# Optimization experiments

Measured on AMD Instinct MI355X. Metric: run time of the kernel, lower is better.

## Reference

```python
import jax, jax.numpy as jnp
import numpy as np

N = 20000        # total nodes
E = 240000       # directed edges (avg in-degree 12); self-loops appended in reference
G = 50           # graphs in the batch
NPG = N // G     # nodes per graph
TD = 768         # text embedding dim
HC = 64          # hidden_channels
H = 8            # attention heads for conv1..conv3 (conv4 uses 1 head)
FD = 3 * HC * H + HC  # JK cat dim for num_layers=4
NEG = 0.2        # GATv2 leaky_relu negative slope
EPS = 1e-5       # GraphNorm eps


def setup_inputs() -> dict:
    key = jax.random.key(0)
    ks = iter(jax.random.split(key, 64))

    def w(shape, s=0.05):
        return jax.random.normal(next(ks), shape, dtype=jnp.float32) * s

    z = lambda *s: jnp.zeros(s, jnp.float32)
    o = lambda *s: jnp.ones(s, jnp.float32)

    inp = {
        'x': w((N, TD), 1.0),
        'edge_index': jax.random.randint(next(ks), (2, E), 0, N, dtype=jnp.int32),
        'batch': jnp.arange(N, dtype=jnp.int32) // NPG,
        'ptr': jnp.arange(G + 1, dtype=jnp.int32) * NPG,
        'tp_w': w((TD, HC)), 'tp_b': z(HC),
        'lin_w': w((FD, 1), 0.005), 'lin_b': z(1),
    }
    # GATv2Conv params: lin_l (source), lin_r (target), att, output bias
    for name, ind, heads, concat in [('c1', HC, H, True), ('c2', HC * H, H, True),
                                     ('c3', HC * H, H, True), ('c4', HC * H, 1, False)]:
        inp[name + '_wl'] = w((ind, heads * HC)); inp[name + '_bl'] = z(heads * HC)
        inp[name + '_wr'] = w((ind, heads * HC)); inp[name + '_br'] = z(heads * HC)
        inp[name + '_att'] = w((heads, HC))
        inp[name + '_bias'] = z(heads * HC if concat else HC)
    # GraphNorm params: weight, bias, mean_scale
    for name, d in [('n1', HC * H), ('n2', HC * H), ('n3', HC * H), ('n4', HC)]:
        inp[name + '_w'] = o(d); inp[name + '_b'] = z(d); inp[name + '_ms'] = o(d)
    return inp


def _gatv2(x, src, dst, wl, bl, wr, br, att, bias, heads, concat):
    # GATv2: e_ij = att . leaky_relu(W_l x_j + W_r x_i); alpha = softmax over in-neighbors of i
    xl = (x @ wl + bl).reshape(N, heads, HC)
    xr = (x @ wr + br).reshape(N, heads, HC)
    e = jax.nn.leaky_relu(xl[src] + xr[dst], NEG)           # [E', H, C]
    logit = jnp.einsum('ehc,hc->eh', e, att)                # [E', H]
    m = jax.ops.segment_max(logit, dst, num_segments=N)     # stable scatter-softmax
    p = jnp.exp(logit - m[dst])
    alpha = p / jax.ops.segment_sum(p, dst, num_segments=N)[dst]
    out = jax.ops.segment_sum(xl[src] * alpha[..., None], dst, num_segments=N)
    out = out.reshape(N, heads * HC) if concat else out.mean(axis=1)
    return out + bias


def _gnorm(x, batch, w, b, ms):
    # PyG GraphNorm: per-graph mean (scaled by mean_scale), per-graph std
    cnt = jax.ops.segment_sum(jnp.ones((N,), x.dtype), batch, num_segments=G)[:, None]
    mean = jax.ops.segment_sum(x, batch, num_segments=G) / cnt
    cen = x - ms * mean[batch]
    var = jax.ops.segment_sum(cen * cen, batch, num_segments=G) / cnt
    return w * cen / jnp.sqrt(var + EPS)[batch] + b


def reference(x, tp_w, tp_b,
              c1_wl, c1_bl, c1_wr, c1_br, c1_att, c1_bias,
              c2_wl, c2_bl, c2_wr, c2_br, c2_att, c2_bias,
              c3_wl, c3_bl, c3_wr, c3_br, c3_att, c3_bias,
              c4_wl, c4_bl, c4_wr, c4_br, c4_att, c4_bias,
              n1_w, n1_b, n1_ms, n2_w, n2_b, n2_ms,
              n3_w, n3_b, n3_ms, n4_w, n4_b, n4_ms,
              lin_w, lin_b, edge_index, batch, ptr):
    sl = jnp.arange(N, dtype=edge_index.dtype)
    src = jnp.concatenate([edge_index[0], sl])  # add_self_loops=True
    dst = jnp.concatenate([edge_index[1], sl])

    h = x @ tp_w + tp_b                          # text_proj (dropout = identity in eval)
    h = _gatv2(h, src, dst, c1_wl, c1_bl, c1_wr, c1_br, c1_att, c1_bias, H, True)
    h = jax.nn.elu(_gnorm(h, batch, n1_w, n1_b, n1_ms))
    xs = [h]
    h2 = _gatv2(h, src, dst, c2_wl, c2_bl, c2_wr, c2_br, c2_att, c2_bias, H, True)
    h = jax.nn.elu(_gnorm(h2 + h, batch, n2_w, n2_b, n2_ms))
    xs.append(h)
    h3 = _gatv2(h, src, dst, c3_wl, c3_bl, c3_wr, c3_br, c3_att, c3_bias, H, True)
    h = jax.nn.elu(_gnorm(h3 + h, batch, n3_w, n3_b, n3_ms))
    xs.append(h)
    h = _gnorm(_gatv2(h, src, dst, c4_wl, c4_bl, c4_wr, c4_br, c4_att, c4_bias, 1, False),
               batch, n4_w, n4_b, n4_ms)
    xs.append(h)

    xcat = jnp.concatenate(xs, axis=1)           # JumpingKnowledge cat -> [N, FD]
    out = xcat[ptr[:-1]] @ lin_w + lin_b         # summary node per graph -> [G, 1]
    return out.squeeze(-1)                       # num_classes==2 -> squeeze
```

## Files before the change

### kernel.cpp

```cpp
#include <hip/hip_runtime.h>
#include <hip/hip_bf16.h>

#define NEG_SLOPE 0.2f
#define EPSI 1e-5f
#define THR 8.0f

typedef __attribute__((ext_vector_type(8))) short bf16x8;
typedef __attribute__((ext_vector_type(4))) float f32x4;

__device__ __forceinline__ float wred_sum(float v){
#pragma unroll
  for (int o = 32; o > 0; o >>= 1) v += __shfl_xor(v, o);
  return v;
}

__device__ __forceinline__ unsigned short f2bf(float f){
  __hip_bfloat16 h = __float2bfloat16(f);
  return *reinterpret_cast<unsigned short*>(&h);
}
__device__ __forceinline__ float bf2f(unsigned short u){
  return __uint_as_float((unsigned int)u << 16);
}

__device__ __forceinline__ void gload16(const void* g, void* l){
  __builtin_amdgcn_global_load_lds((const __attribute__((address_space(1))) unsigned int*)g,
                                   (__attribute__((address_space(3))) unsigned int*)l, 16, 0, 0);
}

__global__ __launch_bounds__(256) void k_count(const int* __restrict__ ei, int* __restrict__ deg,
                                               int E, int EP){
  int e = blockIdx.x * 256 + threadIdx.x;
  if (e >= EP) return;
  int d = (e < E) ? ei[E + e] : (e - E);
  atomicAdd(&deg[d], 1);
}

__global__ __launch_bounds__(256) void k_scan(const int* __restrict__ deg, int* __restrict__ rowptr, int n){
  __shared__ int part[256];
  int t = threadIdx.x;
  int L = (n + 255) / 256;
  int lo = t * L, hi = min(lo + L, n);
  int s = 0;
  for (int i = lo; i < hi; i++) s += deg[i];
  part[t] = s;
  __syncthreads();
  if (t == 0){
    int acc = 0;
    for (int i = 0; i < 256; i++){ int v = part[i]; part[i] = acc; acc += v; }
  }
  __syncthreads();
  int acc = part[t];
  for (int i = lo; i < hi; i++){ rowptr[i] = acc; acc += deg[i]; }
  if (t == 255) rowptr[n] = acc;
}

__global__ __launch_bounds__(256) void k_copy(const int* __restrict__ a, int* __restrict__ b, int n){
  int i = blockIdx.x * 256 + threadIdx.x;
  if (i < n) b[i] = a[i];
}

__global__ __launch_bounds__(256) void k_fill(const int* __restrict__ ei, int* __restrict__ cursor,
                                              int* __restrict__ srcn, int E, int EP){
  int e = blockIdx.x * 256 + threadIdx.x;
  if (e >= EP) return;
  int s, d;
  if (e < E){ s = ei[e]; d = ei[E + e]; } else { s = d = e - E; }
  int pos = atomicAdd(&cursor[d], 1);
  srcn[pos] = s;
}

__global__ __launch_bounds__(256) void k_cvt_act(const float* __restrict__ in,
                                                 unsigned short* __restrict__ ob, int total4){
  int i = blockIdx.x * 256 + threadIdx.x;
  if (i >= total4) return;
  float4 v = ((const float4*)in)[i];
  ushort4 o;
  o.x = f2bf(v.x); o.y = f2bf(v.y); o.z = f2bf(v.z); o.w = f2bf(v.w);
  ((ushort4*)ob)[i] = o;
}

__global__ __launch_bounds__(256) void k_cvt_wt(const float* __restrict__ W,
                                                unsigned short* __restrict__ Wt,
                                                int K, int Ncol){
  __shared__ float t[32][33];
  int bx = blockIdx.x, by = blockIdx.y;
  int tx = threadIdx.x & 31, ty = threadIdx.x >> 5;
#pragma unroll
  for (int i = 0; i < 4; i++)
    t[ty + i * 8][tx] = W[(size_t)(by * 32 + ty + i * 8) * Ncol + bx * 32 + tx];
  __syncthreads();
#pragma unroll
  for (int i = 0; i < 4; i++)
    Wt[(size_t)(bx * 32 + ty + i * 8) * K + by * 32 + tx] = f2bf(t[tx][ty + i * 8]);
}

__global__ __launch_bounds__(256) void k_catb(const float* __restrict__ a,
                                              const float* __restrict__ b,
                                              float* __restrict__ o, int n){
  int i = blockIdx.x * 256 + threadIdx.x;
  if (i < n) o[i] = a[i];
  else if (i < 2 * n) o[i] = b[i - n];
}

template<int BN>
__global__ __launch_bounds__(256) void k_gemm_mfma_t(const unsigned short* __restrict__ A,
                                                     const unsigned short* __restrict__ Wt,
                                                     const float* __restrict__ bias,
                                                     unsigned short* __restrict__ Cb,
                                                     int M, int K, int Ncol){
  constexpr int NF = BN / 32;
  __shared__ unsigned short As[128 * 32];
  __shared__ unsigned short Bs[BN * 32];
  const int tid = threadIdx.x;
  const int w = tid >> 6, lane = tid & 63;
  const int wr = w >> 1, wc = w & 1;
  const int row0 = blockIdx.y * 128, col0 = blockIdx.x * BN;
  const int lr = lane & 15, lk = lane >> 4;
  const int swz = (lr >> 1) & 3;

  f32x4 acc[4][NF];
#pragma unroll
  for (int i = 0; i < 4; i++)
#pragma unroll
    for (int j = 0; j < NF; j++) acc[i][j] = (f32x4){0.f, 0.f, 0.f, 0.f};

  for (int k0 = 0; k0 < K; k0 += 32){
#pragma unroll
    for (int c = 0; c < 2; c++){
      int g = w * 128 + c * 64 + lane;
      int row = g >> 2, slot = g & 3;
      int kq = slot ^ ((row >> 1) & 3);
      int srow = row0 + row; if (srow >= M) srow = M - 1;
      gload16(&A[(size_t)srow * K + k0 + kq * 8], &As[(size_t)(w * 128 + c * 64) * 8]);
    }
#pragma unroll
    for (int c = 0; c < BN / 64; c++){
      int g = w * BN + c * 64 + lane;
      int col = g >> 2, slot = g & 3;
      int kq = slot ^ ((col >> 1) & 3);
      gload16(&Wt[(size_t)(col0 + col) * K + k0 + kq * 8], &Bs[(size_t)(w * BN + c * 64) * 8]);
    }
    __syncthreads();

    bf16x8 af[4], bf_[NF];
#pragma unroll
    for (int mi = 0; mi < 4; mi++){
      int rl = wr * 64 + mi * 16 + lr;
      af[mi] = *(const bf16x8*)&As[(rl * 4 + (lk ^ swz)) * 8];
    }
#pragma unroll
    for (int ni = 0; ni < NF; ni++){
      int cl = wc * (BN / 2) + ni * 16 + lr;
      bf_[ni] = *(const bf16x8*)&Bs[(cl * 4 + (lk ^ swz)) * 8];
    }
#pragma unroll
    for (int mi = 0; mi < 4; mi++)
#pragma unroll
      for (int ni = 0; ni < NF; ni++)
        acc[mi][ni] = __builtin_amdgcn_mfma_f32_16x16x32_bf16(af[mi], bf_[ni], acc[mi][ni], 0, 0, 0);
    __syncthreads();
  }

#pragma unroll
  for (int mi = 0; mi < 4; mi++){
#pragma unroll
    for (int ni = 0; ni < NF; ni++){
      int gc = col0 + wc * (BN / 2) + ni * 16 + lr;
      float bv = bias[gc];
#pragma unroll
      for (int r = 0; r < 4; r++){
        int gr = row0 + wr * 64 + mi * 16 + lk * 4 + r;
        if (gr < M) Cb[(size_t)gr * Ncol + gc] = f2bf(acc[mi][ni][r] + bv);
      }
    }
  }
}

__global__ __launch_bounds__(256) void k_gat_fused8(const unsigned short* __restrict__ xlrb,
                                                    const float* __restrict__ att,
                                                    const int* __restrict__ rowptr,
                                                    const int* __restrict__ srcn,
                                                    const float* __restrict__ bias,
                                                    const unsigned short* __restrict__ resb,
                                                    float* __restrict__ out,
                                                    int N){
  int node = (blockIdx.x * 256 + threadIdx.x) >> 6;
  int lane = threadIdx.x & 63;
  if (node >= N) return;
  float xr[8], av[8];
  {
    bf16x8 r8 = *(const bf16x8*)&xlrb[(size_t)node * 1024 + 512 + lane * 8];
    float4 a0 = *(const float4*)&att[lane * 8];
    float4 a1 = *(const float4*)&att[lane * 8 + 4];
#pragma unroll
    for (int j = 0; j < 8; j++) xr[j] = bf2f((unsigned short)r8[j]);
    av[0] = a0.x; av[1] = a0.y; av[2] = a0.z; av[3] = a0.w;
    av[4] = a1.x; av[5] = a1.y; av[6] = a1.z; av[7] = a1.w;
  }
  int e0 = rowptr[node], e1 = rowptr[node + 1];
  float m0 = -1e30f, s0 = 0.f, m1 = -1e30f, s1 = 0.f;
  float acc0[8] = {}, acc1[8] = {};

  for (int base = e0; base < e1; base += 64){
    int cnt = min(64, e1 - base);
    int sn = 0;
    if (lane < cnt) sn = srcn[base + lane];
    int k = 0;
    for (; k + 1 < cnt; k += 2){
      int ska = __shfl(sn, k);
      int skb = __shfl(sn, k + 1);
      bf16x8 va8 = *(const bf16x8*)&xlrb[(size_t)ska * 1024 + lane * 8];
      bf16x8 vb8 = *(const bf16x8*)&xlrb[(size_t)skb * 1024 + lane * 8];
      float va[8], vb[8];
#pragma unroll
      for (int j = 0; j < 8; j++){ va[j] = bf2f((unsigned short)va8[j]); vb[j] = bf2f((unsigned short)vb8[j]); }
      float suma = 0.f, sumb = 0.f;
#pragma unroll
      for (int j = 0; j < 8; j++){
        float ta = va[j] + xr[j]; ta = ta > 0.f ? ta : NEG_SLOPE * ta; suma += ta * av[j];
        float tb = vb[j] + xr[j]; tb = tb > 0.f ? tb : NEG_SLOPE * tb; sumb += tb * av[j];
      }
      suma += __shfl_xor(suma, 1); sumb += __shfl_xor(sumb, 1);
      suma += __shfl_xor(suma, 2); sumb += __shfl_xor(sumb, 2);
      suma += __shfl_xor(suma, 4); sumb += __shfl_xor(sumb, 4);
      if (__builtin_expect(__any(suma > m0 + THR), 0)){
        float mn = fmaxf(m0, suma);
        float cs = __expf(m0 - mn);
        float p  = __expf(suma - mn);
        s0 = s0 * cs + p;
#pragma unroll
        for (int j = 0; j < 8; j++) acc0[j] = acc0[j] * cs + p * va[j];
        m0 = mn;
      } else {
        float p = __expf(suma - m0);
        s0 += p;
#pragma unroll
        for (int j = 0; j < 8; j++) acc0[j] += p * va[j];
      }
      if (__builtin_expect(__any(sumb > m1 + THR), 0)){
        float mn = fmaxf(m1, sumb);
        float cs = __expf(m1 - mn);
        float p  = __expf(sumb - mn);
        s1 = s1 * cs + p;
#pragma unroll
        for (int j = 0; j < 8; j++) acc1[j] = acc1[j] * cs + p * vb[j];
        m1 = mn;
      } else {
        float p = __expf(sumb - m1);
        s1 += p;
#pragma unroll
        for (int j = 0; j < 8; j++) acc1[j] += p * vb[j];
      }
    }
    if (k < cnt){
      int ska = __shfl(sn, k);
      bf16x8 va8 = *(const bf16x8*)&xlrb[(size_t)ska * 1024 + lane * 8];
      float va[8];
#pragma unroll
      for (int j = 0; j < 8; j++) va[j] = bf2f((unsigned short)va8[j]);
      float suma = 0.f;
#pragma unroll
      for (int j = 0; j < 8; j++){
        float ta = va[j] + xr[j]; ta = ta > 0.f ? ta : NEG_SLOPE * ta; suma += ta * av[j];
      }
      suma += __shfl_xor(suma, 1);
      suma += __shfl_xor(suma, 2);
      suma += __shfl_xor(suma, 4);
      if (__builtin_expect(__any(suma > m0 + THR), 0)){
        float mn = fmaxf(m0, suma);
        float cs = __expf(m0 - mn);
        float p  = __expf(suma - mn);
        s0 = s0 * cs + p;
#pragma unroll
        for (int j = 0; j < 8; j++) acc0[j] = acc0[j] * cs + p * va[j];
        m0 = mn;
      } else {
        float p = __expf(suma - m0);
        s0 += p;
#pragma unroll
        for (int j = 0; j < 8; j++) acc0[j] += p * va[j];
      }
    }
  }
  float m = fmaxf(m0, m1);
  float c0 = __expf(m0 - m), c1 = __expf(m1 - m);
  float s = s0 * c0 + s1 * c1;
  float inv = 1.f / s;
  size_t o = (size_t)node * 512 + lane * 8;
  float4 bv0 = *(const float4*)&bias[lane * 8];
  float4 bv1 = *(const float4*)&bias[lane * 8 + 4];
  float rr[8] = {};
  if (resb){
    bf16x8 r8 = *(const bf16x8*)&resb[o];
#pragma unroll
    for (int j = 0; j < 8; j++) rr[j] = bf2f((unsigned short)r8[j]);
  }
  float bb[8] = {bv0.x, bv0.y, bv0.z, bv0.w, bv1.x, bv1.y, bv1.z, bv1.w};
  float4 o0, o1;
  float res8[8];
#pragma unroll
  for (int j = 0; j < 8; j++)
    res8[j] = (acc0[j] * c0 + acc1[j] * c1) * inv + bb[j] + rr[j];
  o0.x = res8[0]; o0.y = res8[1]; o0.z = res8[2]; o0.w = res8[3];
  o1.x = res8[4]; o1.y = res8[5]; o1.z = res8[6]; o1.w = res8[7];
  *(float4*)&out[o] = o0;
  *(float4*)&out[o + 4] = o1;
}

__global__ __launch_bounds__(256) void k_gat_fused1(const unsigned short* __restrict__ xlr,
                                                    const float* __restrict__ att,
                                                    const int* __restrict__ rowptr,
                                                    const int* __restrict__ srcn,
                                                    const float* __restrict__ bias,
                                                    float* __restrict__ out,
                                                    int N){
  int node = (blockIdx.x * 256 + threadIdx.x) >> 6;
  int lane = threadIdx.x & 63;
  if (node >= N) return;
  float xrv = bf2f(xlr[(size_t)node * 128 + 64 + lane]);
  float attv = att[lane];
  int e0 = rowptr[node], e1 = rowptr[node + 1];
  float m = -1e30f, s = 0.f, acc = 0.f;
  for (int base = e0; base < e1; base += 64){
    int cnt = min(64, e1 - base);
    int sn = 0;
    if (lane < cnt) sn = srcn[base + lane];
    for (int k = 0; k < cnt; k++){
      int sk = __shfl(sn, k);
      float v = bf2f(xlr[(size_t)sk * 128 + lane]);
      float t = v + xrv;
      t = t > 0.f ? t : NEG_SLOPE * t;
      float sum = wred_sum(t * attv);
      if (sum > m + THR){
        float mn = fmaxf(m, sum);
        float cs = __expf(m - mn);
        float p  = __expf(sum - mn);
        s = s * cs + p;
        acc = acc * cs + p * v;
        m = mn;
      } else {
        float p = __expf(sum - m);
        s += p;
        acc += p * v;
      }
    }
  }
  out[(size_t)node * 64 + lane] = acc / s + bias[lane];
}

#define NCHUNK 16
__global__ __launch_bounds__(256) void k_gnorm_stats(const float* __restrict__ y,
                                                     const int* __restrict__ ptrg,
                                                     float* __restrict__ psum,
                                                     float* __restrict__ psq,
                                                     int OD){
  int g = blockIdx.x, chunk = blockIdx.z;
  int lane = threadIdx.x & 63, sub = threadIdx.x >> 6;
  int c = blockIdx.y * 64 + lane;
  int lo = ptrg[g], hi = ptrg[g + 1], len = hi - lo;
  int c0 = lo + (len * chunk) / NCHUNK, c1 = lo + (len * (chunk + 1)) / NCHUNK;
  float s = 0.f, q = 0.f;
  for (int i = c0 + sub; i < c1; i += 4){
    float v = y[(size_t)i * OD + c];
    s += v; q += v * v;
  }
  __shared__ float sm[4][64], sq2[4][64];
  sm[sub][lane] = s; sq2[sub][lane] = q;
  __syncthreads();
  if (sub == 0){
    s = sm[0][lane] + sm[1][lane] + sm[2][lane] + sm[3][lane];
    q = sq2[0][lane] + sq2[1][lane] + sq2[2][lane] + sq2[3][lane];
    size_t o = (size_t)(g * NCHUNK + chunk) * OD + c;
    psum[o] = s; psq[o] = q;
  }
}

__global__ __launch_bounds__(256) void k_gnorm_coef(const float* __restrict__ psum,
                                                    const float* __restrict__ psq,
                                                    const float* __restrict__ w,
                                                    const float* __restrict__ b,
                                                    const float* __restrict__ ms,
                                                    const int* __restrict__ ptrg,
                                                    float* __restrict__ cA,
                                                    float* __restrict__ cC,
                                                    int OD){
  int g = blockIdx.x;
  int len = ptrg[g + 1] - ptrg[g];
  float inv_n = 1.f / (float)len;
  for (int c = threadIdx.x; c < OD; c += 256){
    float s = 0.f, q = 0.f;
    for (int k = 0; k < NCHUNK; k++){
      size_t o = (size_t)(g * NCHUNK + k) * OD + c;
      s += psum[o]; q += psq[o];
    }
    float mean = s * inv_n, ey2 = q * inv_n;
    float m = ms[c];
    float var = ey2 - mean * mean * (2.f * m - m * m);
    float inv = rsqrtf(var + EPSI);
    float A = w[c] * inv;
    cA[(size_t)g * OD + c] = A;
    cC[(size_t)g * OD + c] = b[c] - A * m * mean;
  }
}

__global__ __launch_bounds__(256) void k_gnorm_apply(const float* __restrict__ y,
                                                     const int* __restrict__ batch,
                                                     const float* __restrict__ cA,
                                                     const float* __restrict__ cC,
                                                     unsigned short* __restrict__ outb,
                                                     int OD, int total4, int do_elu){
  int idx = blockIdx.x * 256 + threadIdx.x;
  if (idx >= total4) return;
  int od4 = OD >> 2;
  int node = idx / od4;
  int c = (idx - node * od4) << 2;
  int g = batch[node];
  float4 v = ((const float4*)y)[idx];
  float4 A = *(const float4*)&cA[(size_t)g * OD + c];
  float4 Cc = *(const float4*)&cC[(size_t)g * OD + c];
  float4 r;
  r.x = A.x * v.x + Cc.x;
  r.y = A.y * v.y + Cc.y;
  r.z = A.z * v.z + Cc.z;
  r.w = A.w * v.w + Cc.w;
  if (do_elu){
    r.x = r.x > 0.f ? r.x : expf(r.x) - 1.f;
    r.y = r.y > 0.f ? r.y : expf(r.y) - 1.f;
    r.z = r.z > 0.f ? r.z : expf(r.z) - 1.f;
    r.w = r.w > 0.f ? r.w : expf(r.w) - 1.f;
  }
  ushort4 ob;
  ob.x = f2bf(r.x); ob.y = f2bf(r.y); ob.z = f2bf(r.z); ob.w = f2bf(r.w);
  ((ushort4*)outb)[idx] = ob;
}

__global__ __launch_bounds__(64) void k_extract(const unsigned short* __restrict__ srcb,
                                                float* __restrict__ cat,
                                                const int* __restrict__ ptrg,
                                                int OD, int off, int FD){
  int g = blockIdx.x;
  int c = blockIdx.y * 64 + threadIdx.x;
  cat[(size_t)g * FD + off + c] = bf2f(srcb[(size_t)ptrg[g] * OD + c]);
}

__global__ __launch_bounds__(256) void k_final(const float* __restrict__ cat,
                                               const float* __restrict__ lin_w,
                                               const float* __restrict__ lin_b,
                                               float* __restrict__ out, int FD){
  int g = blockIdx.x;
  float s = 0.f;
  for (int c = threadIdx.x; c < FD; c += 256) s += cat[(size_t)g * FD + c] * lin_w[c];
  s = wred_sum(s);
  __shared__ float sm[4];
  if ((threadIdx.x & 63) == 0) sm[threadIdx.x >> 6] = s;
  __syncthreads();
  if (threadIdx.x == 0) out[g] = sm[0] + sm[1] + sm[2] + sm[3] + lin_b[0];
}

extern "C" void kernel_launch(void* const* d_in, const int* in_sizes, int n_in,
                              void* d_out, int out_size, void* d_ws, size_t ws_size,
                              hipStream_t stream) {
  const int TD = 768, HC = 64, H = 8;
  const float* x     = (const float*)d_in[0];
  const int*   ei    = (const int*)d_in[1];
  const int*   batch = (const int*)d_in[2];
  const int*   ptrg  = (const int*)d_in[3];
  const float* tp_w  = (const float*)d_in[4];
  const float* tp_b  = (const float*)d_in[5];
  const float* lin_w = (const float*)d_in[6];
  const float* lin_b = (const float*)d_in[7];
  const float* cw[4][6];
  for (int l = 0; l < 4; l++)
    for (int j = 0; j < 6; j++) cw[l][j] = (const float*)d_in[8 + 6 * l + j];
  const float* nw[4][3];
  for (int l = 0; l < 4; l++)
    for (int j = 0; j < 3; j++) nw[l][j] = (const float*)d_in[32 + 3 * l + j];

  const int N  = in_sizes[0] / TD;
  const int E  = in_sizes[1] / 2;
  const int EP = E + N;
  const int G  = in_sizes[3] - 1;
  const int FD = 3 * HC * H + HC;

  char* wsp = (char*)d_ws;
  size_t off = 0;
  auto alloc = [&](size_t b) -> void* {
    void* p = wsp + off;
    off += (b + 255) & ~(size_t)255;
    return p;
  };
  float* tmpF  = (float*)alloc((size_t)N * 512 * 4);
  unsigned short* xlrb = (unsigned short*)alloc((size_t)N * 1024 * 2);
  unsigned short* actA = (unsigned short*)alloc((size_t)N * 512 * 2);
  unsigned short* h0h  = (unsigned short*)alloc((size_t)N * 64 * 2);
  int*   rowptr= (int*)alloc((size_t)(N + 1) * 4);
  int*   cursor= (int*)alloc((size_t)N * 4);
  int*   srcn  = (int*)alloc((size_t)EP * 4);
  float* cat   = (float*)alloc((size_t)G * FD * 4);
  float* psum  = (float*)alloc((size_t)G * NCHUNK * 512 * 4);
  float* psq   = (float*)alloc((size_t)G * NCHUNK * 512 * 4);
  float* cA    = (float*)alloc((size_t)G * 512 * 4);
  float* cC    = (float*)alloc((size_t)G * 512 * 4);
  unsigned short* WtLR = (unsigned short*)alloc((size_t)1024 * 512 * 2);
  unsigned short* WtTP = (unsigned short*)alloc((size_t)64 * 768 * 2);
  unsigned short* Wt4  = (unsigned short*)alloc((size_t)128 * 512 * 2);
  float* cbias = (float*)alloc(1024 * 4);
  (void)ws_size; (void)n_in; (void)out_size;

  float* out = (float*)d_out;

  unsigned short* xbf   = xlrb;
  unsigned short* xlr4b = xlrb;
  float* agg4 = tmpF;

  hipMemsetAsync(cursor, 0, (size_t)N * 4, stream);
  int eblk = (EP + 255) / 256;
  k_count<<<eblk, 256, 0, stream>>>(ei, cursor, E, EP);
  k_scan<<<1, 256, 0, stream>>>(cursor, rowptr, N);
  k_copy<<<(N + 255) / 256, 256, 0, stream>>>(rowptr, cursor, N);
  k_fill<<<eblk, 256, 0, stream>>>(ei, cursor, srcn, E, EP);

  const int mfmaRows = (N + 127) / 128;
  const int nodeBlocks = (N + 3) / 4;

  k_cvt_act<<<(N * TD / 4 + 255) / 256, 256, 0, stream>>>(x, xbf, N * TD / 4);
  k_cvt_wt<<<dim3(2, TD / 32), 256, 0, stream>>>(tp_w, WtTP, TD, 64);
  k_gemm_mfma_t<64><<<dim3(1, mfmaRows), 256, 0, stream>>>(xbf, WtTP, tp_b, h0h, N, TD, 64);

  auto layer8 = [&](const unsigned short* actbf, int Kin, int l,
                    const unsigned short* resb, unsigned short* youtb, int catoff){
    k_cvt_wt<<<dim3(16, Kin / 32), 256, 0, stream>>>(cw[l][0], WtLR, Kin, 512);
    k_cvt_wt<<<dim3(16, Kin / 32), 256, 0, stream>>>(cw[l][2], WtLR + (size_t)512 * Kin, Kin, 512);
    k_catb<<<4, 256, 0, stream>>>(cw[l][1], cw[l][3], cbias, 512);
    k_gemm_mfma_t<128><<<dim3(8, mfmaRows), 256, 0, stream>>>(actbf, WtLR, cbias, xlrb, N, Kin, 1024);
    k_gat_fused8<<<nodeBlocks, 256, 0, stream>>>(xlrb, cw[l][4], rowptr, srcn,
                                                 cw[l][5], resb, tmpF, N);
    k_gnorm_stats<<<dim3(G, 8, NCHUNK), 256, 0, stream>>>(tmpF, ptrg, psum, psq, 512);
    k_gnorm_coef<<<G, 256, 0, stream>>>(psum, psq, nw[l][0], nw[l][1], nw[l][2], ptrg, cA, cC, 512);
    int total4 = N * 128;
    k_gnorm_apply<<<(total4 + 255) / 256, 256, 0, stream>>>(tmpF, batch, cA, cC, youtb,
                                                            512, total4, 1);
    k_extract<<<dim3(G, 8), 64, 0, stream>>>(youtb, cat, ptrg, 512, catoff, FD);
  };

  layer8(h0h,  64,  0, nullptr, actA, 0);
  layer8(actA, 512, 1, actA,    actA, 512);
  layer8(actA, 512, 2, actA,    actA, 1024);

  k_cvt_wt<<<dim3(2, 16), 256, 0, stream>>>(cw[3][0], Wt4, 512, 64);
  k_cvt_wt<<<dim3(2, 16), 256, 0, stream>>>(cw[3][2], Wt4 + (size_t)64 * 512, 512, 64);
  k_catb<<<1, 256, 0, stream>>>(cw[3][1], cw[3][3], cbias, 64);
  k_gemm_mfma_t<64><<<dim3(2, mfmaRows), 256, 0, stream>>>(actA, Wt4, cbias, xlr4b, N, 512, 128);
  k_gat_fused1<<<nodeBlocks, 256, 0, stream>>>(xlr4b, cw[3][4], rowptr, srcn,
                                               cw[3][5], agg4, N);
  k_gnorm_stats<<<dim3(G, 1, NCHUNK), 256, 0, stream>>>(agg4, ptrg, psum, psq, 64);
  k_gnorm_coef<<<G, 256, 0, stream>>>(psum, psq, nw[3][0], nw[3][1], nw[3][2], ptrg, cA, cC, 64);
  k_gnorm_apply<<<(N * 16 + 255) / 256, 256, 0, stream>>>(agg4, batch, cA, cC, h0h,
                                                          64, N * 16, 0);
  k_extract<<<dim3(G, 1), 64, 0, stream>>>(h0h, cat, ptrg, 64, 1536, FD);

  k_final<<<G, 256, 0, stream>>>(cat, lin_w, lin_b, out, FD);
}
```

Measured before the change: 551.2 us.

## Store GAT outputs in bf16, fuse small kernels, widen GEMM tiles, pack math

The GAT aggregation output now goes to bf16 instead of fp32, which halves the traffic through the GraphNorm stats and apply passes. Several small launches are removed: the k_copy pass is folded into the scan, the two weight conversions and the bias concat are merged, and the summary-node extract is folded into gnorm apply. The GEMM moves to 512-thread blocks with wider N tiles and reads its two biases directly. The GAT inner loop uses packed float2 math and a max-based leaky ReLU. Rounding the pre-norm activations to bf16 adds precision loss before the normalization statistics are computed.

```diff
diff --git a/kernel.cpp b/kernel.cpp
--- a/kernel.cpp
+++ b/kernel.cpp
@@ -7,6 +7,7 @@
 
 typedef __attribute__((ext_vector_type(8))) short bf16x8;
 typedef __attribute__((ext_vector_type(4))) float f32x4;
+typedef __attribute__((ext_vector_type(2))) float f32x2;
 
 __device__ __forceinline__ float wred_sum(float v){
 #pragma unroll
@@ -20,6 +21,19 @@
 }
 __device__ __forceinline__ float bf2f(unsigned short u){
   return __uint_as_float((unsigned int)u << 16);
+}
+__device__ __forceinline__ f32x2 bfpair(unsigned int u){
+  f32x2 r;
+  r.x = __uint_as_float(u << 16);
+  r.y = __uint_as_float(u & 0xffff0000u);
+  return r;
+}
+__device__ __forceinline__ f32x2 vmax2(f32x2 a, f32x2 b){
+#if __has_builtin(__builtin_elementwise_max)
+  return __builtin_elementwise_max(a, b);
+#else
+  f32x2 r; r.x = fmaxf(a.x, b.x); r.y = fmaxf(a.y, b.y); return r;
+#endif
 }
 
 __device__ __forceinline__ void gload16(const void* g, void* l){
@@ -35,7 +49,7 @@
   atomicAdd(&deg[d], 1);
 }
 
-__global__ __launch_bounds__(256) void k_scan(const int* __restrict__ deg, int* __restrict__ rowptr, int n){
+__global__ __launch_bounds__(256) void k_scan(int* __restrict__ deg, int* __restrict__ rowptr, int n){
   __shared__ int part[256];
   int t = threadIdx.x;
   int L = (n + 255) / 256;
@@ -50,13 +64,13 @@
   }
   __syncthreads();
   int acc = part[t];
-  for (int i = lo; i < hi; i++){ rowptr[i] = acc; acc += deg[i]; }
+  for (int i = lo; i < hi; i++){
+    int d = deg[i];
+    rowptr[i] = acc;
+    deg[i] = acc;
+    acc += d;
+  }
   if (t == 255) rowptr[n] = acc;
-}
-
-__global__ __launch_bounds__(256) void k_copy(const int* __restrict__ a, int* __restrict__ b, int n){
-  int i = blockIdx.x * 256 + threadIdx.x;
-  if (i < n) b[i] = a[i];
 }
 
 __global__ __launch_bounds__(256) void k_fill(const int* __restrict__ ei, int* __restrict__ cursor,
@@ -94,26 +108,41 @@
     Wt[(size_t)(bx * 32 + ty + i * 8) * K + by * 32 + tx] = f2bf(t[tx][ty + i * 8]);
 }
 
-__global__ __launch_bounds__(256) void k_catb(const float* __restrict__ a,
-                                              const float* __restrict__ b,
-                                              float* __restrict__ o, int n){
-  int i = blockIdx.x * 256 + threadIdx.x;
-  if (i < n) o[i] = a[i];
-  else if (i < 2 * n) o[i] = b[i - n];
+__global__ __launch_bounds__(256) void k_cvt_wt2(const float* __restrict__ Wa,
+                                                 const float* __restrict__ Wb,
+                                                 unsigned short* __restrict__ Wt,
+                                                 int K, int Ncol){
+  __shared__ float t[32][33];
+  int half = gridDim.x >> 1;
+  int isB = blockIdx.x >= half;
+  const float* W = isB ? Wb : Wa;
+  unsigned short* out = Wt + (isB ? (size_t)Ncol * K : 0);
+  int bx = isB ? blockIdx.x - half : blockIdx.x;
+  int by = blockIdx.y;
+  int tx = threadIdx.x & 31, ty = threadIdx.x >> 5;
+#pragma unroll
+  for (int i = 0; i < 4; i++)
+    t[ty + i * 8][tx] = W[(size_t)(by * 32 + ty + i * 8) * Ncol + bx * 32 + tx];
+  __syncthreads();
+#pragma unroll
+  for (int i = 0; i < 4; i++)
+    out[(size_t)(bx * 32 + ty + i * 8) * K + by * 32 + tx] = f2bf(t[tx][ty + i * 8]);
 }
 
 template<int BN>
-__global__ __launch_bounds__(256) void k_gemm_mfma_t(const unsigned short* __restrict__ A,
-                                                     const unsigned short* __restrict__ Wt,
-                                                     const float* __restrict__ bias,
-                                                     unsigned short* __restrict__ Cb,
-                                                     int M, int K, int Ncol){
-  constexpr int NF = BN / 32;
+__global__ __launch_bounds__(512) void k_gemm_mfma8(const unsigned short* __restrict__ A,
+                                                    const unsigned short* __restrict__ Wt,
+                                                    const float* __restrict__ ba,
+                                                    const float* __restrict__ bb,
+                                                    int bsplit,
+                                                    unsigned short* __restrict__ Cb,
+                                                    int M, int K, int Ncol){
+  constexpr int NF = BN / 64;
   __shared__ unsigned short As[128 * 32];
   __shared__ unsigned short Bs[BN * 32];
   const int tid = threadIdx.x;
   const int w = tid >> 6, lane = tid & 63;
-  const int wr = w >> 1, wc = w & 1;
+  const int wr = w >> 2, wc = w & 3;
   const int row0 = blockIdx.y * 128, col0 = blockIdx.x * BN;
   const int lr = lane & 15, lk = lane >> 4;
   const int swz = (lr >> 1) & 3;
@@ -125,20 +154,18 @@
     for (int j = 0; j < NF; j++) acc[i][j] = (f32x4){0.f, 0.f, 0.f, 0.f};
 
   for (int k0 = 0; k0 < K; k0 += 32){
-#pragma unroll
-    for (int c = 0; c < 2; c++){
-      int g = w * 128 + c * 64 + lane;
+    for (int g0 = w * 64; g0 < 512; g0 += 512){
+      int g = g0 + lane;
       int row = g >> 2, slot = g & 3;
       int kq = slot ^ ((row >> 1) & 3);
       int srow = row0 + row; if (srow >= M) srow = M - 1;
-      gload16(&A[(size_t)srow * K + k0 + kq * 8], &As[(size_t)(w * 128 + c * 64) * 8]);
-    }
-#pragma unroll
-    for (int c = 0; c < BN / 64; c++){
-      int g = w * BN + c * 64 + lane;
+      gload16(&A[(size_t)srow * K + k0 + kq * 8], &As[(size_t)g0 * 8]);
+    }
+    for (int g0 = w * 64; g0 < BN * 4; g0 += 512){
+      int g = g0 + lane;
       int col = g >> 2, slot = g & 3;
       int kq = slot ^ ((col >> 1) & 3);
-      gload16(&Wt[(size_t)(col0 + col) * K + k0 + kq * 8], &Bs[(size_t)(w * BN + c * 64) * 8]);
+      gload16(&Wt[(size_t)(col0 + col) * K + k0 + kq * 8], &Bs[(size_t)g0 * 8]);
     }
     __syncthreads();
 
@@ -150,7 +177,7 @@
     }
 #pragma unroll
     for (int ni = 0; ni < NF; ni++){
-      int cl = wc * (BN / 2) + ni * 16 + lr;
+      int cl = wc * (BN / 4) + ni * 16 + lr;
       bf_[ni] = *(const bf16x8*)&Bs[(cl * 4 + (lk ^ swz)) * 8];
     }
 #pragma unroll
@@ -165,8 +192,8 @@
   for (int mi = 0; mi < 4; mi++){
 #pragma unroll
     for (int ni = 0; ni < NF; ni++){
-      int gc = col0 + wc * (BN / 2) + ni * 16 + lr;
-      float bv = bias[gc];
+      int gc = col0 + wc * (BN / 4) + ni * 16 + lr;
+      float bv = gc < bsplit ? ba[gc] : bb[gc - bsplit];
 #pragma unroll
       for (int r = 0; r < 4; r++){
         int gr = row0 + wr * 64 + mi * 16 + lk * 4 + r;
@@ -182,24 +209,23 @@
                                                     const int* __restrict__ srcn,
                                                     const float* __restrict__ bias,
                                                     const unsigned short* __restrict__ resb,
-                                                    float* __restrict__ out,
+                                                    unsigned short* __restrict__ yb,
                                                     int N){
   int node = (blockIdx.x * 256 + threadIdx.x) >> 6;
   int lane = threadIdx.x & 63;
   if (node >= N) return;
-  float xr[8], av[8];
+  f32x2 xr2[4], av2[4];
   {
-    bf16x8 r8 = *(const bf16x8*)&xlrb[(size_t)node * 1024 + 512 + lane * 8];
+    uint4 ur = *(const uint4*)&xlrb[(size_t)node * 1024 + 512 + lane * 8];
+    xr2[0] = bfpair(ur.x); xr2[1] = bfpair(ur.y); xr2[2] = bfpair(ur.z); xr2[3] = bfpair(ur.w);
     float4 a0 = *(const float4*)&att[lane * 8];
     float4 a1 = *(const float4*)&att[lane * 8 + 4];
-#pragma unroll
-    for (int j = 0; j < 8; j++) xr[j] = bf2f((unsigned short)r8[j]);
-    av[0] = a0.x; av[1] = a0.y; av[2] = a0.z; av[3] = a0.w;
-    av[4] = a1.x; av[5] = a1.y; av[6] = a1.z; av[7] = a1.w;
+    av2[0] = (f32x2){a0.x, a0.y}; av2[1] = (f32x2){a0.z, a0.w};
+    av2[2] = (f32x2){a1.x, a1.y}; av2[3] = (f32x2){a1.z, a1.w};
   }
   int e0 = rowptr[node], e1 = rowptr[node + 1];
   float m0 = -1e30f, s0 = 0.f, m1 = -1e30f, s1 = 0.f;
-  float acc0[8] = {}, acc1[8] = {};
+  f32x2 acc0[4] = {}, acc1[4] = {};
 
   for (int base = e0; base < e1; base += 64){
     int cnt = min(64, e1 - base);
@@ -209,17 +235,22 @@
     for (; k + 1 < cnt; k += 2){
       int ska = __shfl(sn, k);
       int skb = __shfl(sn, k + 1);
-      bf16x8 va8 = *(const bf16x8*)&xlrb[(size_t)ska * 1024 + lane * 8];
-      bf16x8 vb8 = *(const bf16x8*)&xlrb[(size_t)skb * 1024 + lane * 8];
-      float va[8], vb[8];
-#pragma unroll
-      for (int j = 0; j < 8; j++){ va[j] = bf2f((unsigned short)va8[j]); vb[j] = bf2f((unsigned short)vb8[j]); }
-      float suma = 0.f, sumb = 0.f;
-#pragma unroll
-      for (int j = 0; j < 8; j++){
-        float ta = va[j] + xr[j]; ta = ta > 0.f ? ta : NEG_SLOPE * ta; suma += ta * av[j];
-        float tb = vb[j] + xr[j]; tb = tb > 0.f ? tb : NEG_SLOPE * tb; sumb += tb * av[j];
-      }
+      uint4 ua = *(const uint4*)&xlrb[(size_t)ska * 1024 + lane * 8];
+      uint4 ub = *(const uint4*)&xlrb[(size_t)skb * 1024 + lane * 8];
+      f32x2 va[4], vb[4];
+      va[0] = bfpair(ua.x); va[1] = bfpair(ua.y); va[2] = bfpair(ua.z); va[3] = bfpair(ua.w);
+      vb[0] = bfpair(ub.x); vb[1] = bfpair(ub.y); vb[2] = bfpair(ub.z); vb[3] = bfpair(ub.w);
+      f32x2 da = (f32x2){0.f, 0.f}, db = (f32x2){0.f, 0.f};
+#pragma unroll
+      for (int j = 0; j < 4; j++){
+        f32x2 ta = va[j] + xr2[j];
+        f32x2 tb = vb[j] + xr2[j];
+        ta = vmax2(ta, ta * NEG_SLOPE);
+        tb = vmax2(tb, tb * NEG_SLOPE);
+        da += ta * av2[j];
+        db += tb * av2[j];
+      }
+      float suma = da.x + da.y, sumb = db.x + db.y;
       suma += __shfl_xor(suma, 1); sumb += __shfl_xor(sumb, 1);
       suma += __shfl_xor(suma, 2); sumb += __shfl_xor(sumb, 2);
       suma += __shfl_xor(suma, 4); sumb += __shfl_xor(sumb, 4);
@@ -229,13 +260,13 @@
         float p  = __expf(suma - mn);
         s0 = s0 * cs + p;
 #pragma unroll
-        for (int j = 0; j < 8; j++) acc0[j] = acc0[j] * cs + p * va[j];
+        for (int j = 0; j < 4; j++) acc0[j] = acc0[j] * cs + va[j] * p;
         m0 = mn;
       } else {
         float p = __expf(suma - m0);
         s0 += p;
 #pragma unroll
-        for (int j = 0; j < 8; j++) acc0[j] += p * va[j];
+        for (int j = 0; j < 4; j++) acc0[j] += va[j] * p;
       }
       if (__builtin_expect(__any(sumb > m1 + THR), 0)){
         float mn = fmaxf(m1, sumb);
@@ -243,26 +274,28 @@
         float p  = __expf(sumb - mn);
         s1 = s1 * cs + p;
 #pragma unroll
-        for (int j = 0; j < 8; j++) acc1[j] = acc1[j] * cs + p * vb[j];
+        for (int j = 0; j < 4; j++) acc1[j] = acc1[j] * cs + vb[j] * p;
         m1 = mn;
       } else {
         float p = __expf(sumb - m1);
         s1 += p;
 #pragma unroll
-        for (int j = 0; j < 8; j++) acc1[j] += p * vb[j];
+        for (int j = 0; j < 4; j++) acc1[j] += vb[j] * p;
       }
     }
     if (k < cnt){
       int ska = __shfl(sn, k);
-      bf16x8 va8 = *(const bf16x8*)&xlrb[(size_t)ska * 1024 + lane * 8];
-      float va[8];
-#pragma unroll
-      for (int j = 0; j < 8; j++) va[j] = bf2f((unsigned short)va8[j]);
-      float suma = 0.f;
-#pragma unroll
-      for (int j = 0; j < 8; j++){
-        float ta = va[j] + xr[j]; ta = ta > 0.f ? ta : NEG_SLOPE * ta; suma += ta * av[j];
-      }
+      uint4 ua = *(const uint4*)&xlrb[(size_t)ska * 1024 + lane * 8];
+      f32x2 va[4];
+      va[0] = bfpair(ua.x); va[1] = bfpair(ua.y); va[2] = bfpair(ua.z); va[3] = bfpair(ua.w);
+      f32x2 da = (f32x2){0.f, 0.f};
+#pragma unroll
+      for (int j = 0; j < 4; j++){
+        f32x2 ta = va[j] + xr2[j];
+        ta = vmax2(ta, ta * NEG_SLOPE);
+        da += ta * av2[j];
+      }
+      float suma = da.x + da.y;
       suma += __shfl_xor(suma, 1);
       suma += __shfl_xor(suma, 2);
       suma += __shfl_xor(suma, 4);
@@ -272,13 +305,13 @@
         float p  = __expf(suma - mn);
         s0 = s0 * cs + p;
 #pragma unroll
-        for (int j = 0; j < 8; j++) acc0[j] = acc0[j] * cs + p * va[j];
+        for (int j = 0; j < 4; j++) acc0[j] = acc0[j] * cs + va[j] * p;
         m0 = mn;
       } else {
         float p = __expf(suma - m0);
         s0 += p;
 #pragma unroll
-        for (int j = 0; j < 8; j++) acc0[j] += p * va[j];
+        for (int j = 0; j < 4; j++) acc0[j] += va[j] * p;
       }
     }
   }
@@ -286,25 +319,24 @@
   float c0 = __expf(m0 - m), c1 = __expf(m1 - m);
   float s = s0 * c0 + s1 * c1;
   float inv = 1.f / s;
+  float4 b0 = *(const float4*)&bias[lane * 8];
+  float4 b1 = *(const float4*)&bias[lane * 8 + 4];
+  f32x2 bi2[4] = {(f32x2){b0.x, b0.y}, (f32x2){b0.z, b0.w},
+                  (f32x2){b1.x, b1.y}, (f32x2){b1.z, b1.w}};
+  f32x2 re2[4] = {};
   size_t o = (size_t)node * 512 + lane * 8;
-  float4 bv0 = *(const float4*)&bias[lane * 8];
-  float4 bv1 = *(const float4*)&bias[lane * 8 + 4];
-  float rr[8] = {};
   if (resb){
-    bf16x8 r8 = *(const bf16x8*)&resb[o];
-#pragma unroll
-    for (int j = 0; j < 8; j++) rr[j] = bf2f((unsigned short)r8[j]);
-  }
-  float bb[8] = {bv0.x, bv0.y, bv0.z, bv0.w, bv1.x, bv1.y, bv1.z, bv1.w};
-  float4 o0, o1;
-  float res8[8];
-#pragma unroll
-  for (int j = 0; j < 8; j++)
-    res8[j] = (acc0[j] * c0 + acc1[j] * c1) * inv + bb[j] + rr[j];
-  o0.x = res8[0]; o0.y = res8[1]; o0.z = res8[2]; o0.w = res8[3];
-  o1.x = res8[4]; o1.y = res8[5]; o1.z = res8[6]; o1.w = res8[7];
-  *(float4*)&out[o] = o0;
-  *(float4*)&out[o + 4] = o1;
+    uint4 rr = *(const uint4*)&resb[o];
+    re2[0] = bfpair(rr.x); re2[1] = bfpair(rr.y); re2[2] = bfpair(rr.z); re2[3] = bfpair(rr.w);
+  }
+  bf16x8 ov;
+#pragma unroll
+  for (int j = 0; j < 4; j++){
+    f32x2 r = (acc0[j] * c0 + acc1[j] * c1) * inv + bi2[j] + re2[j];
+    ov[2 * j]     = (short)f2bf(r.x);
+    ov[2 * j + 1] = (short)f2bf(r.y);
+  }
+  *(bf16x8*)&yb[o] = ov;
 }
 
 __global__ __launch_bounds__(256) void k_gat_fused1(const unsigned short* __restrict__ xlr,
@@ -312,7 +344,7 @@
                                                     const int* __restrict__ rowptr,
                                                     const int* __restrict__ srcn,
                                                     const float* __restrict__ bias,
-                                                    float* __restrict__ out,
+                                                    unsigned short* __restrict__ yb4,
                                                     int N){
   int node = (blockIdx.x * 256 + threadIdx.x) >> 6;
   int lane = threadIdx.x & 63;
@@ -329,7 +361,7 @@
       int sk = __shfl(sn, k);
       float v = bf2f(xlr[(size_t)sk * 128 + lane]);
       float t = v + xrv;
-      t = t > 0.f ? t : NEG_SLOPE * t;
+      t = fmaxf(t, t * NEG_SLOPE);
       float sum = wred_sum(t * attv);
       if (sum > m + THR){
         float mn = fmaxf(m, sum);
@@ -345,11 +377,11 @@
       }
     }
   }
-  out[(size_t)node * 64 + lane] = acc / s + bias[lane];
+  yb4[(size_t)node * 64 + lane] = f2bf(acc / s + bias[lane]);
 }
 
 #define NCHUNK 16
-__global__ __launch_bounds__(256) void k_gnorm_stats(const float* __restrict__ y,
+__global__ __launch_bounds__(256) void k_gnorm_stats(const unsigned short* __restrict__ y,
                                                      const int* __restrict__ ptrg,
                                                      float* __restrict__ psum,
                                                      float* __restrict__ psq,
@@ -361,7 +393,7 @@
   int c0 = lo + (len * chunk) / NCHUNK, c1 = lo + (len * (chunk + 1)) / NCHUNK;
   float s = 0.f, q = 0.f;
   for (int i = c0 + sub; i < c1; i += 4){
-    float v = y[(size_t)i * OD + c];
+    float v = bf2f(y[(size_t)i * OD + c]);
     s += v; q += v * v;
   }
   __shared__ float sm[4][64], sq2[4][64];
@@ -403,11 +435,14 @@
   }
 }
 
-__global__ __launch_bounds__(256) void k_gnorm_apply(const float* __restrict__ y,
+__global__ __launch_bounds__(256) void k_gnorm_apply(const unsigned short* __restrict__ y,
                                                      const int* __restrict__ batch,
                                                      const float* __restrict__ cA,
                                                      const float* __restrict__ cC,
                                                      unsigned short* __restrict__ outb,
+                                                     const int* __restrict__ ptrg,
+                                                     float* __restrict__ cat,
+                                                     int catoff, int FD,
                                                      int OD, int total4, int do_elu){
   int idx = blockIdx.x * 256 + threadIdx.x;
   if (idx >= total4) return;
@@ -415,7 +450,8 @@
   int node = idx / od4;
   int c = (idx - node * od4) << 2;
   int g = batch[node];
-  float4 v = ((const float4*)y)[idx];
+  ushort4 uv = ((const ushort4*)y)[idx];
+  float4 v = make_float4(bf2f(uv.x), bf2f(uv.y), bf2f(uv.z), bf2f(uv.w));
   float4 A = *(const float4*)&cA[(size_t)g * OD + c];
   float4 Cc = *(const float4*)&cC[(size_t)g * OD + c];
   float4 r;
@@ -432,15 +468,8 @@
   ushort4 ob;
   ob.x = f2bf(r.x); ob.y = f2bf(r.y); ob.z = f2bf(r.z); ob.w = f2bf(r.w);
   ((ushort4*)outb)[idx] = ob;
-}
-
-__global__ __launch_bounds__(64) void k_extract(const unsigned short* __restrict__ srcb,
-                                                float* __restrict__ cat,
-                                                const int* __restrict__ ptrg,
-                                                int OD, int off, int FD){
-  int g = blockIdx.x;
-  int c = blockIdx.y * 64 + threadIdx.x;
-  cat[(size_t)g * FD + off + c] = bf2f(srcb[(size_t)ptrg[g] * OD + c]);
+  if (node == ptrg[g])
+    *(float4*)&cat[(size_t)g * FD + catoff + c] = r;
 }
 
 __global__ __launch_bounds__(256) void k_final(const float* __restrict__ cat,
@@ -489,8 +518,8 @@
     off += (b + 255) & ~(size_t)255;
     return p;
   };
-  float* tmpF  = (float*)alloc((size_t)N * 512 * 4);
   unsigned short* xlrb = (unsigned short*)alloc((size_t)N * 1024 * 2);
+  unsigned short* yb   = (unsigned short*)alloc((size_t)N * 512 * 2);
   unsigned short* actA = (unsigned short*)alloc((size_t)N * 512 * 2);
   unsigned short* h0h  = (unsigned short*)alloc((size_t)N * 64 * 2);
   int*   rowptr= (int*)alloc((size_t)(N + 1) * 4);
@@ -504,20 +533,18 @@
   unsigned short* WtLR = (unsigned short*)alloc((size_t)1024 * 512 * 2);
   unsigned short* WtTP = (unsigned short*)alloc((size_t)64 * 768 * 2);
   unsigned short* Wt4  = (unsigned short*)alloc((size_t)128 * 512 * 2);
-  float* cbias = (float*)alloc(1024 * 4);
   (void)ws_size; (void)n_in; (void)out_size;
 
   float* out = (float*)d_out;
 
   unsigned short* xbf   = xlrb;
   unsigned short* xlr4b = xlrb;
-  float* agg4 = tmpF;
+  unsigned short* yb4   = yb;
 
   hipMemsetAsync(cursor, 0, (size_t)N * 4, stream);
   int eblk = (EP + 255) / 256;
   k_count<<<eblk, 256, 0, stream>>>(ei, cursor, E, EP);
   k_scan<<<1, 256, 0, stream>>>(cursor, rowptr, N);
-  k_copy<<<(N + 255) / 256, 256, 0, stream>>>(rowptr, cursor, N);
   k_fill<<<eblk, 256, 0, stream>>>(ei, cursor, srcn, E, EP);
 
   const int mfmaRows = (N + 127) / 128;
@@ -525,39 +552,37 @@
 
   k_cvt_act<<<(N * TD / 4 + 255) / 256, 256, 0, stream>>>(x, xbf, N * TD / 4);
   k_cvt_wt<<<dim3(2, TD / 32), 256, 0, stream>>>(tp_w, WtTP, TD, 64);
-  k_gemm_mfma_t<64><<<dim3(1, mfmaRows), 256, 0, stream>>>(xbf, WtTP, tp_b, h0h, N, TD, 64);
+  k_gemm_mfma8<64><<<dim3(1, mfmaRows), 512, 0, stream>>>(xbf, WtTP, tp_b, tp_b, 64, h0h, N, TD, 64);
 
   auto layer8 = [&](const unsigned short* actbf, int Kin, int l,
-                    const unsigned short* resb, unsigned short* youtb, int catoff){
-    k_cvt_wt<<<dim3(16, Kin / 32), 256, 0, stream>>>(cw[l][0], WtLR, Kin, 512);
-    k_cvt_wt<<<dim3(16, Kin / 32), 256, 0, stream>>>(cw[l][2], WtLR + (size_t)512 * Kin, Kin, 512);
-    k_catb<<<4, 256, 0, stream>>>(cw[l][1], cw[l][3], cbias, 512);
-    k_gemm_mfma_t<128><<<dim3(8, mfmaRows), 256, 0, stream>>>(actbf, WtLR, cbias, xlrb, N, Kin, 1024);
+                    const unsigned short* resb, int catoff){
+    k_cvt_wt2<<<dim3(32, Kin / 32), 256, 0, stream>>>(cw[l][0], cw[l][2], WtLR, Kin, 512);
+    k_gemm_mfma8<256><<<dim3(4, mfmaRows), 512, 0, stream>>>(actbf, WtLR, cw[l][1], cw[l][3], 512,
+                                                             xlrb, N, Kin, 1024);
     k_gat_fused8<<<nodeBlocks, 256, 0, stream>>>(xlrb, cw[l][4], rowptr, srcn,
-                                                 cw[l][5], resb, tmpF, N);
-    k_gnorm_stats<<<dim3(G, 8, NCHUNK), 256, 0, stream>>>(tmpF, ptrg, psum, psq, 512);
+                                                 cw[l][5], resb, yb, N);
+    k_gnorm_stats<<<dim3(G, 8, NCHUNK), 256, 0, stream>>>(yb, ptrg, psum, psq, 512);
     k_gnorm_coef<<<G, 256, 0, stream>>>(psum, psq, nw[l][0], nw[l][1], nw[l][2], ptrg, cA, cC, 512);
     int total4 = N * 128;
-    k_gnorm_apply<<<(total4 + 255) / 256, 256, 0, stream>>>(tmpF, batch, cA, cC, youtb,
+    k_gnorm_apply<<<(total4 + 255) / 256, 256, 0, stream>>>(yb, batch, cA, cC, actA,
+                                                            ptrg, cat, catoff, FD,
                                                             512, total4, 1);
-    k_extract<<<dim3(G, 8), 64, 0, stream>>>(youtb, cat, ptrg, 512, catoff, FD);
   };
 
-  layer8(h0h,  64,  0, nullptr, actA, 0);
-  layer8(actA, 512, 1, actA,    actA, 512);
-  layer8(actA, 512, 2, actA,    actA, 1024);
-
-  k_cvt_wt<<<dim3(2, 16), 256, 0, stream>>>(cw[3][0], Wt4, 512, 64);
-  k_cvt_wt<<<dim3(2, 16), 256, 0, stream>>>(cw[3][2], Wt4 + (size_t)64 * 512, 512, 64);
-  k_catb<<<1, 256, 0, stream>>>(cw[3][1], cw[3][3], cbias, 64);
-  k_gemm_mfma_t<64><<<dim3(2, mfmaRows), 256, 0, stream>>>(actA, Wt4, cbias, xlr4b, N, 512, 128);
+  layer8(h0h,  64,  0, nullptr, 0);
+  layer8(actA, 512, 1, actA,    512);
+  layer8(actA, 512, 2, actA,    1024);
+
+  k_cvt_wt2<<<dim3(4, 16), 256, 0, stream>>>(cw[3][0], cw[3][2], Wt4, 512, 64);
+  k_gemm_mfma8<128><<<dim3(1, mfmaRows), 512, 0, stream>>>(actA, Wt4, cw[3][1], cw[3][3], 64,
+                                                           xlr4b, N, 512, 128);
   k_gat_fused1<<<nodeBlocks, 256, 0, stream>>>(xlr4b, cw[3][4], rowptr, srcn,
-                                               cw[3][5], agg4, N);
-  k_gnorm_stats<<<dim3(G, 1, NCHUNK), 256, 0, stream>>>(agg4, ptrg, psum, psq, 64);
+                                               cw[3][5], yb4, N);
+  k_gnorm_stats<<<dim3(G, 1, NCHUNK), 256, 0, stream>>>(yb4, ptrg, psum, psq, 64);
   k_gnorm_coef<<<G, 256, 0, stream>>>(psum, psq, nw[3][0], nw[3][1], nw[3][2], ptrg, cA, cC, 64);
-  k_gnorm_apply<<<(N * 16 + 255) / 256, 256, 0, stream>>>(agg4, batch, cA, cC, h0h,
+  k_gnorm_apply<<<(N * 16 + 255) / 256, 256, 0, stream>>>(yb4, batch, cA, cC, h0h,
+                                                          ptrg, cat, 1536, FD,
                                                           64, N * 16, 0);
-  k_extract<<<dim3(G, 1), 64, 0, stream>>>(h0h, cat, ptrg, 64, 1536, FD);
 
   k_final<<<G, 256, 0, stream>>>(cat, lin_w, lin_b, out, FD);
 }
```

New measurement: 507.6 us. 1.09x faster.
